# Performance work log

Measured on AMD Instinct MI355X. Metric: run time of the kernel, lower is better.

## Reference

```python
import jax, jax.numpy as jnp
import numpy as np

DIM = 384
NHEAD = 8
HD = DIM // NHEAD          # 48, rotary/pos-enc head dim
P = 3
CORR_DIM = 2 * 49 * P * P  # 882
NFRAMES = 24
PPI = 96                   # patches per frame
NPATCH = NFRAMES * PPI     # 2304 SoftAgg segments (unique kk)
E = NPATCH * NFRAMES       # 55296 edges
M = PPI                    # tokens per (i,j) group


def _linear(x, W, b):
    return x @ W + b


def _ln(x, g, b, eps=1e-3):
    mu = x.mean(-1, keepdims=True)
    var = ((x - mu) ** 2).mean(-1, keepdims=True)
    return (x - mu) * jax.lax.rsqrt(var + eps) * g + b


def _mlp2(x, W1, b1, W2, b2):
    return _linear(jax.nn.relu(_linear(x, W1, b1)), W2, b2)


@jax.custom_vjp
def grad_clip(x):
    return x

def _gc_fwd(x):
    return x, None

def _gc_bwd(_, g):
    g = jnp.where(jnp.isnan(g), jnp.zeros_like(g), g)
    return (jnp.clip(g, -0.01, 0.01),)

grad_clip.defvjp(_gc_fwd, _gc_bwd)


def _soft_agg(x, seg, Wf, bf, Wg, bg, Wh, bh):
    # x: [1,E,D]; seg: [E] contiguous segment ids in [0, NPATCH)
    g = _linear(x, Wg, bg)[0]                                    # [E,D]
    gmax = jax.ops.segment_max(g, seg, num_segments=NPATCH)
    ex = jnp.exp(g - gmax[seg])
    den = jax.ops.segment_sum(ex, seg, num_segments=NPATCH)
    w = ex / den[seg]                                            # scatter_softmax over segments
    f = _linear(x, Wf, bf)[0]
    y = jax.ops.segment_sum(f * w, seg, num_segments=NPATCH)     # [NPATCH,D]
    return _linear(y, Wh, bh)[seg][None]                         # expand back to [1,E,D]


def _rotate_half(x):
    x1, x2 = jnp.split(x, 2, axis=-1)
    return jnp.concatenate([-x2, x1], axis=-1)


def _gated_linear_attention(x, cos, sin, Wq, bq, Wk, bk, Wv, bv, Wm, bm, Wgt, bgt):
    # x: [N,M,D]; cos/sin: [N,1,M,HD] broadcast over heads
    N = x.shape[0]
    def heads(t):
        return t.reshape(N, M, NHEAD, HD).transpose(0, 2, 1, 3)  # [N,H,M,HD]
    q = heads(_linear(x, Wq, bq))
    k = heads(_linear(x, Wk, bk))
    v = heads(_linear(x, Wv, bv))
    q = q * cos + _rotate_half(q) * sin
    k = k * cos + _rotate_half(k) * sin
    Q = jax.nn.elu(q) + 1.0
    K = jax.nn.elu(k) + 1.0
    KV = jnp.einsum('nhsd,nhsv->nhdv', K, v)
    Z = 1.0 / (jnp.einsum('nhld,nhd->nhl', Q, K.sum(2)) + 1e-6)
    out = jnp.einsum('nhld,nhdv,nhl->nhlv', Q, KV, Z)
    msg = _linear(out.transpose(0, 2, 1, 3).reshape(N, M, DIM), Wm, bm)
    gate = jax.nn.sigmoid(_linear(jnp.concatenate([x, msg], -1), Wgt, bgt))
    return x + gate * msg


def _forward(net, inp, corr, posenc_cache, kk, ix, jx, ij_ind,
             Wc1, bc1, Wc2, bc2, g_lnc, b_lnc, Wc3, bc3,
             g_norm, b_norm,
             W1a, b1a, W1b, b1b, W2a, b2a, W2b, b2b,
             Wf, bf, Wg, bg, Wh, bh,
             g_norm2, b_norm2,
             Wq, bq, Wk, bk, Wv, bv, Wm, bm, Wgt, bgt,
             Wd, bd, Ww, bw):
    # corr encoder: Linear-ReLU-Linear-LN-ReLU-Linear
    c = jax.nn.relu(_linear(corr, Wc1, bc1))
    c = _ln(_linear(c, Wc2, bc2), g_lnc, b_lnc)
    c = _linear(jax.nn.relu(c), Wc3, bc3)
    net = net + inp + c
    net = _ln(net, g_norm, b_norm)
    # neighbor gather + masked MLP + residual (mask applied BEFORE the MLP, as in torch)
    mask_ix = (ix >= 0).astype(net.dtype)[None, :, None]
    mask_jx = (jx >= 0).astype(net.dtype)[None, :, None]
    net = net + _mlp2(mask_ix * net[:, ix], W1a, b1a, W1b, b1b)
    net = net + _mlp2(mask_jx * net[:, jx], W2a, b2a, W2b, b2b)
    net = net + _soft_agg(net, kk, Wf, bf, Wg, bg, Wh, bh)
    b = net.shape[0]
    flat = ij_ind.reshape(-1)
    tokens = net[:, flat, :].reshape(-1, M, DIM)                 # [N,M,D], N = E//M
    pe = posenc_cache[:, :, :, flat, :].reshape(2, tokens.shape[0], 1, M, HD)
    tokens = _ln(tokens, g_norm2, b_norm2)
    tokens = _gated_linear_attention(tokens, pe[0], pe[1], Wq, bq, Wk, bk, Wv, bv, Wm, bm, Wgt, bgt)
    tokens = tokens.reshape(b, -1, DIM)
    reverse_ind = jnp.zeros((E,), jnp.int32).at[flat].set(jnp.arange(E, dtype=jnp.int32))
    net = tokens[:, reverse_ind, :]
    d_out = grad_clip(_linear(jax.nn.relu(net), Wd, bd))
    w_out = jax.nn.sigmoid(grad_clip(_linear(jax.nn.relu(net), Ww, bw)))
    return net, d_out, w_out


def setup_inputs() -> dict:
    key = jax.random.key(0)
    ki = iter(jax.random.split(key, 80))
    # complete patch graph: each patch connects to all frames; edge id = k*NFRAMES + j
    kkn = np.repeat(np.arange(NPATCH), NFRAMES)
    iin = kkn // PPI
    jjn = np.tile(np.arange(NFRAMES), NPATCH)
    e = np.arange(E)
    ixn = np.where(jjn >= 1, e - 1, -1)                 # fastba.neighbors: same kk, jj-1
    jxn = np.where(jjn + 1 < NFRAMES, e + 1, -1)        # same kk, jj+1
    ij = iin * 12345 + jjn
    ij_ind = np.sort(np.argsort(ij, kind='stable').reshape(-1, M), axis=-1)

    def rn(shape):
        return jax.random.normal(next(ki), shape, jnp.float32)
    def W(fi, fo):
        s = 1.0 / np.sqrt(fi)
        return jax.random.uniform(next(ki), (fi, fo), jnp.float32, -s, s)
    def bvec(fi, n):
        s = 1.0 / np.sqrt(fi)
        return jax.random.uniform(next(ki), (n,), jnp.float32, -s, s)

    theta = jax.random.uniform(next(ki), (1, 1, E, HD), jnp.float32, 0.0, 2.0 * np.pi)
    posenc = jnp.stack([jnp.cos(theta), jnp.sin(theta)], axis=0)  # [2,1,1,E,HD]

    return {
        'net': rn((1, E, DIM)), 'inp': rn((1, E, DIM)),
        'corr': rn((1, E, CORR_DIM)), 'flow': rn((1, E, 2)),
        'posenc_cache': posenc,
        'ii': jnp.asarray(iin, jnp.int32), 'jj': jnp.asarray(jjn, jnp.int32),
        'kk': jnp.asarray(kkn, jnp.int32), 'ix': jnp.asarray(ixn, jnp.int32),
        'jx': jnp.asarray(jxn, jnp.int32), 'ij_ind': jnp.asarray(ij_ind, jnp.int32),
        'Wc1': W(CORR_DIM, DIM), 'bc1': bvec(CORR_DIM, DIM),
        'Wc2': W(DIM, DIM), 'bc2': bvec(DIM, DIM),
        'g_lnc': jnp.ones((DIM,), jnp.float32), 'b_lnc': jnp.zeros((DIM,), jnp.float32),
        'Wc3': W(DIM, DIM), 'bc3': bvec(DIM, DIM),
        'g_norm': jnp.ones((DIM,), jnp.float32), 'b_norm': jnp.zeros((DIM,), jnp.float32),
        'W1a': W(DIM, DIM), 'b1a': bvec(DIM, DIM), 'W1b': W(DIM, DIM), 'b1b': bvec(DIM, DIM),
        'W2a': W(DIM, DIM), 'b2a': bvec(DIM, DIM), 'W2b': W(DIM, DIM), 'b2b': bvec(DIM, DIM),
        'Wf': W(DIM, DIM), 'bf': bvec(DIM, DIM), 'Wg': W(DIM, DIM), 'bg': bvec(DIM, DIM),
        'Wh': W(DIM, DIM), 'bh': bvec(DIM, DIM),
        'g_norm2': jnp.ones((DIM,), jnp.float32), 'b_norm2': jnp.zeros((DIM,), jnp.float32),
        'Wq': W(DIM, DIM), 'bq': bvec(DIM, DIM), 'Wk': W(DIM, DIM), 'bk': bvec(DIM, DIM),
        'Wv': W(DIM, DIM), 'bv': bvec(DIM, DIM), 'Wm': W(DIM, DIM), 'bm': bvec(DIM, DIM),
        'Wgt': W(2 * DIM, DIM), 'bgt': bvec(2 * DIM, DIM),
        'Wd': W(DIM, 2), 'bd': bvec(DIM, 2), 'Ww': W(DIM, 2), 'bw': bvec(DIM, 2),
    }


def reference(net, inp, corr, flow, posenc_cache, ii, jj, kk, ix, jx, ij_ind,
              Wc1, bc1, Wc2, bc2, g_lnc, b_lnc, Wc3, bc3,
              g_norm, b_norm,
              W1a, b1a, W1b, b1b, W2a, b2a, W2b, b2b,
              Wf, bf, Wg, bg, Wh, bh,
              g_norm2, b_norm2,
              Wq, bq, Wk, bk, Wv, bv, Wm, bm, Wgt, bgt,
              Wd, bd, Ww, bw):
    return _forward(net, inp, corr, posenc_cache, kk, ix, jx, ij_ind,
                    Wc1, bc1, Wc2, bc2, g_lnc, b_lnc, Wc3, bc3,
                    g_norm, b_norm,
                    W1a, b1a, W1b, b1b, W2a, b2a, W2b, b2b,
                    Wf, bf, Wg, bg, Wh, bh,
                    g_norm2, b_norm2,
                    Wq, bq, Wk, bk, Wv, bv, Wm, bm, Wgt, bgt,
                    Wd, bd, Ww, bw)
```

## Files before the change

### kernel.cpp

```cpp
#include <hip/hip_runtime.h>
#include <math.h>

#define DIMV 384
#define NHEADV 8
#define HDV 48
#define CORR_DIMV 882
#define CORR_PAD 896
#define NFRAMESV 24
#define PPIV 96
#define NPATCHV (NFRAMESV * PPIV)
#define ETOK (NPATCHV * NFRAMESV)
#define MTOK 96
#define NGRP (ETOK / MTOK)

using f32x4 = __attribute__((ext_vector_type(4))) float;
using s16x8 = __attribute__((ext_vector_type(8))) short;
using u16x4 = __attribute__((ext_vector_type(4))) unsigned short;

__device__ __forceinline__ unsigned int f2bf(float x) {
    union { float f; unsigned int u; } c; c.f = x;
    unsigned int u = c.u;
    u += 0x7fffu + ((u >> 16) & 1u);
    return u >> 16;
}
__device__ __forceinline__ float bf2f(unsigned short x) {
    union { unsigned int u; float f; } c; c.u = ((unsigned int)x) << 16;
    return c.f;
}

__device__ __forceinline__ void gload_lds16(const void* g, void* l) {
    __builtin_amdgcn_global_load_lds(
        (const __attribute__((address_space(1))) unsigned int*)g,
        (__attribute__((address_space(3))) unsigned int*)l, 16, 0, 0);
}

__device__ __forceinline__ void xcd_tile(int& colblk, int& rowblk) {
    const int nwg  = gridDim.x * gridDim.y;
    const int flat = blockIdx.y * gridDim.x + blockIdx.x;
    const int xcd  = flat & 7;
    const int base = flat >> 3;
    const int q = nwg >> 3, r = nwg & 7;
    const int nf = (xcd < r ? xcd * (q + 1) : r * (q + 1) + (xcd - r) * q) + base;
    colblk = nf % gridDim.x;
    rowblk = nf / gridDim.x;
}

template<int EPI, bool GATHER>
__global__ __launch_bounds__(256)
void gemm_bb(const unsigned short* __restrict__ A, int lda,
             const unsigned short* __restrict__ Wt,
             const float* __restrict__ bias,
             float* __restrict__ C,
             unsigned short* __restrict__ Cb, int ldcb, int cbofs,
             const int* __restrict__ gidx,
             const unsigned short* __restrict__ zrow, int K)
{
    int colblk, rowblk;
    xcd_tile(colblk, rowblk);
    const int row0 = rowblk * 128;
    const int col0 = colblk * 128;

    __shared__ __align__(16) unsigned short As[2 * 128 * 32];
    __shared__ __align__(16) unsigned short Bs[2 * 128 * 32];

    const int tid  = threadIdx.x;
    const int lane = tid & 63;
    const int wid  = tid >> 6;
    const int wm   = wid >> 1;
    const int wn   = wid & 1;

    const int rl = lane >> 2;
    const int cp = lane & 3;

    const unsigned short* asrc[2];
    const unsigned short* bsrc[2];
    #pragma unroll
    for (int s = 0; s < 2; ++s) {
        const int r = wid * 32 + s * 16 + rl;
        const int c = cp ^ ((r >> 1) & 3);
        long arow = row0 + r;
        if (GATHER) arow = gidx[row0 + r];
        asrc[s] = (GATHER && arow < 0) ? (zrow + c * 8)
                                       : (A + arow * (long)lda + c * 8);
        bsrc[s] = Wt + (long)(col0 + r) * K + c * 8;
    }

    f32x4 acc[4][4] = {};
    const int ntiles = K >> 5;
    const int rsel = lane & 15;
    const int kq   = lane >> 4;

    auto stage = [&](int b, int ko) {
        unsigned short* a0 = &As[b * 4096 + wid * 1024];
        unsigned short* b0 = &Bs[b * 4096 + wid * 1024];
        gload_lds16(asrc[0] + ko, a0);
        gload_lds16(asrc[1] + ko, a0 + 512);
        gload_lds16(bsrc[0] + ko, b0);
        gload_lds16(bsrc[1] + ko, b0 + 512);
    };
    auto body = [&](int b) {
        const unsigned short* Ab = &As[b * 4096];
        const unsigned short* Bf = &Bs[b * 4096];
        s16x8 a[4], w[4];
        #pragma unroll
        for (int i = 0; i < 4; ++i) {
            const int R = wm * 64 + i * 16 + rsel;
            a[i] = *(const s16x8*)&Ab[R * 32 + ((kq ^ ((R >> 1) & 3)) << 3)];
        }
        #pragma unroll
        for (int j = 0; j < 4; ++j) {
            const int R = wn * 64 + j * 16 + rsel;
            w[j] = *(const s16x8*)&Bf[R * 32 + ((kq ^ ((R >> 1) & 3)) << 3)];
        }
        #pragma unroll
        for (int i = 0; i < 4; ++i)
            #pragma unroll
            for (int j = 0; j < 4; ++j)
                acc[i][j] = __builtin_amdgcn_mfma_f32_16x16x32_bf16(a[i], w[j], acc[i][j], 0, 0, 0);
    };

    stage(0, 0);
    int cur = 0;
    for (int t = 0; t + 1 < ntiles; ++t) {
        stage(cur ^ 1, (t + 1) << 5);
        asm volatile("s_waitcnt vmcnt(4)\n\ts_barrier" ::: "memory");
        body(cur);
        asm volatile("s_barrier" ::: "memory");
        cur ^= 1;
    }
    asm volatile("s_waitcnt vmcnt(0)\n\ts_barrier" ::: "memory");
    body(cur);

    const int ccol = lane & 15;
    const int rgrp = lane >> 4;
    #pragma unroll
    for (int i = 0; i < 4; ++i) {
        const long rbase = row0 + wm * 64 + i * 16 + rgrp * 4;
        #pragma unroll
        for (int j = 0; j < 4; ++j) {
            const int col = col0 + wn * 64 + j * 16 + ccol;
            const float bsv = bias ? bias[col] : 0.f;
            #pragma unroll
            for (int rr = 0; rr < 4; ++rr) {
                const long row = rbase + rr;
                float v = acc[i][j][rr] + bsv;
                if (EPI == 0) C[row * (long)DIMV + col] = v;
                if (EPI == 1) Cb[row * (long)ldcb + cbofs + col] = (unsigned short)f2bf(fmaxf(v, 0.f));
                if (EPI == 5) Cb[row * (long)ldcb + cbofs + col] = (unsigned short)f2bf(v);
                if (EPI == 6) { const long off = row * (long)ldcb + col;
                                Cb[off] = (unsigned short)f2bf(bf2f(Cb[off]) + v); }
                if (EPI == 7) {
                    const float gate = 1.f / (1.f + expf(-v));
                    const float tok  = bf2f(Cb[row * (long)ldcb + col]);
                    const float msg  = bf2f(Cb[row * (long)ldcb + cbofs + col]);
                    C[(long)gidx[row] * DIMV + col] = tok + gate * msg;
                }
            }
        }
    }
}

struct WPtrs13 { const float* p[13]; };

__global__ __launch_bounds__(256)
void wtrans13(WPtrs13 w, unsigned short* __restrict__ out)
{
    __shared__ float t[32][33];
    const float* W = w.p[blockIdx.z];
    unsigned short* O = out + (size_t)blockIdx.z * DIMV * DIMV;
    const int k0 = blockIdx.x * 32, n0 = blockIdx.y * 32;
    const int tx = threadIdx.x, ty = threadIdx.y;
    #pragma unroll
    for (int i = ty; i < 32; i += 8)
        t[i][tx] = W[(long)(k0 + i) * DIMV + n0 + tx];
    __syncthreads();
    #pragma unroll
    for (int i = ty; i < 32; i += 8)
        O[(long)(n0 + i) * DIMV + k0 + tx] = (unsigned short)f2bf(t[tx][i]);
}

__global__ __launch_bounds__(256)
void wtransb(const float* __restrict__ W, unsigned short* __restrict__ O,
             int krows, int ldo)
{
    __shared__ float t[32][33];
    const int k0 = blockIdx.x * 32, n0 = blockIdx.y * 32;
    const int tx = threadIdx.x, ty = threadIdx.y;
    #pragma unroll
    for (int i = ty; i < 32; i += 8)
        t[i][tx] = (k0 + i < krows) ? W[(long)(k0 + i) * DIMV + n0 + tx] : 0.f;
    __syncthreads();
    #pragma unroll
    for (int i = ty; i < 32; i += 8)
        O[(long)(n0 + i) * ldo + k0 + tx] = (unsigned short)f2bf(t[tx][i]);
}

__global__ __launch_bounds__(256)
void corrconv(const float* __restrict__ corr, unsigned int* __restrict__ corrb,
              unsigned int* __restrict__ zr)
{
    if (blockIdx.x == 0 && threadIdx.x < 512) zr[threadIdx.x] = 0u;
    const long idx = (long)blockIdx.x * 256 + threadIdx.x;
    if (idx >= (long)ETOK * (CORR_PAD / 2)) return;
    const long e = idx / (CORR_PAD / 2);
    const int  p = (int)(idx % (CORR_PAD / 2));
    const int  k = p * 2;
    unsigned v = 0u;
    if (k + 1 < CORR_DIMV) {
        const float2 f = *(const float2*)(corr + e * CORR_DIMV + k);
        v = f2bf(f.x) | (f2bf(f.y) << 16);
    }
    corrb[idx] = v;
}

__global__ __launch_bounds__(256)
void biascat(const float* __restrict__ bq, const float* __restrict__ bk,
             const float* __restrict__ bv, const float* __restrict__ bg,
             const float* __restrict__ bf_, float* __restrict__ bqkv,
             float* __restrict__ bgf)
{
    const int t = blockIdx.x * 256 + threadIdx.x;
    if (t < 384)       { bqkv[t] = bq[t];       bgf[t] = bg[t]; }
    else if (t < 768)  { bqkv[t] = bk[t - 384]; bgf[t] = bf_[t - 384]; }
    else if (t < 1152) { bqkv[t] = bv[t - 768]; }
}

template<int MODE, bool RELUB>
__global__ __launch_bounds__(256)
void ln_kernel(unsigned short* __restrict__ dstb, int ldb,
               const float* __restrict__ s0, const float* __restrict__ s1,
               const unsigned short* __restrict__ sb,
               const float* __restrict__ seg, const int* __restrict__ gather,
               const float* __restrict__ g, const float* __restrict__ b)
{
    const int wave = threadIdx.x >> 6;
    const int lane = threadIdx.x & 63;
    const long row = (long)blockIdx.x * 4 + wave;
    const long srow = (MODE == 2) ? (long)gather[row] : row;

    float x[6];
    float sum = 0.f;
    #pragma unroll
    for (int i = 0; i < 6; ++i) {
        int c = lane + i * 64;
        float v;
        if (MODE == 0) v = bf2f(sb[srow * DIMV + c]);
        if (MODE == 1) v = s0[srow * DIMV + c] + s1[srow * DIMV + c] + bf2f(sb[srow * DIMV + c]);
        if (MODE == 2) v = bf2f(sb[srow * DIMV + c]) + seg[(srow / NFRAMESV) * DIMV + c];
        x[i] = v; sum += v;
    }
    #pragma unroll
    for (int o = 32; o > 0; o >>= 1) sum += __shfl_xor(sum, o);
    float mu = sum * (1.f / DIMV);
    float vs = 0.f;
    #pragma unroll
    for (int i = 0; i < 6; ++i) { float d = x[i] - mu; vs += d * d; }
    #pragma unroll
    for (int o = 32; o > 0; o >>= 1) vs += __shfl_xor(vs, o);
    float rstd = rsqrtf(vs * (1.f / DIMV) + 1e-3f);
    #pragma unroll
    for (int i = 0; i < 6; ++i) {
        int c = lane + i * 64;
        float y = (x[i] - mu) * rstd * g[c] + b[c];
        dstb[row * (long)ldb + c] = (unsigned short)f2bf(RELUB ? fmaxf(y, 0.f) : y);
    }
}

__global__ __launch_bounds__(384)
void softagg_kernel(const unsigned short* __restrict__ gf,
                    unsigned short* __restrict__ yb)
{
    const int p = blockIdx.x;
    const int col = threadIdx.x;
    const long base = (long)p * NFRAMESV * 768 + col;
    float gv[NFRAMESV];
    float gmax = -INFINITY;
    #pragma unroll
    for (int r = 0; r < NFRAMESV; ++r) {
        gv[r] = bf2f(gf[base + (long)r * 768]);
        gmax = fmaxf(gmax, gv[r]);
    }
    float den = 0.f;
    #pragma unroll
    for (int r = 0; r < NFRAMESV; ++r) { gv[r] = expf(gv[r] - gmax); den += gv[r]; }
    float acc = 0.f;
    #pragma unroll
    for (int r = 0; r < NFRAMESV; ++r) acc += bf2f(gf[base + 384 + (long)r * 768]) * gv[r];
    yb[(long)p * DIMV + col] = (unsigned short)f2bf(acc / den);
}

__global__ __launch_bounds__(256)
void rope_kernel(unsigned short* __restrict__ q, unsigned short* __restrict__ k,
                 int ld, const float* __restrict__ pos, const int* __restrict__ flat)
{
    const long idx = (long)blockIdx.x * 256 + threadIdx.x;
    const long e = idx / 48;
    const int rem = (int)(idx % 48);
    const int h = rem / 6, d4 = (rem % 6) * 4;
    const int tok = flat[e];
    const float* cp = pos + (long)tok * HDV;
    const float* sp = pos + (long)ETOK * HDV + (long)tok * HDV;
    const float4 c1 = *(const float4*)(cp + d4);
    const float4 c2 = *(const float4*)(cp + d4 + 24);
    const float4 s1 = *(const float4*)(sp + d4);
    const float4 s2 = *(const float4*)(sp + d4 + 24);
    const long o1 = e * ld + h * HDV + d4;
    const long o2 = o1 + 24;

    float c1a[4] = {c1.x, c1.y, c1.z, c1.w};
    float c2a[4] = {c2.x, c2.y, c2.z, c2.w};
    float s1a[4] = {s1.x, s1.y, s1.z, s1.w};
    float s2a[4] = {s2.x, s2.y, s2.z, s2.w};

    u16x4 q1 = *(const u16x4*)&q[o1];
    u16x4 q2 = *(const u16x4*)&q[o2];
    u16x4 k1 = *(const u16x4*)&k[o1];
    u16x4 k2 = *(const u16x4*)&k[o2];
    u16x4 q1o, q2o, k1o, k2o;
    #pragma unroll
    for (int i = 0; i < 4; ++i) {
        const float qa = bf2f(q1[i]), qb = bf2f(q2[i]);
        float r1 = qa * c1a[i] - qb * s1a[i];
        float r2 = qb * c2a[i] + qa * s2a[i];
        r1 = (r1 > 0.f) ? r1 + 1.f : expf(r1);
        r2 = (r2 > 0.f) ? r2 + 1.f : expf(r2);
        q1o[i] = (unsigned short)f2bf(r1);
        q2o[i] = (unsigned short)f2bf(r2);
        const float ka = bf2f(k1[i]), kb = bf2f(k2[i]);
        float t1 = ka * c1a[i] - kb * s1a[i];
        float t2 = kb * c2a[i] + ka * s2a[i];
        t1 = (t1 > 0.f) ? t1 + 1.f : expf(t1);
        t2 = (t2 > 0.f) ? t2 + 1.f : expf(t2);
        k1o[i] = (unsigned short)f2bf(t1);
        k2o[i] = (unsigned short)f2bf(t2);
    }
    *(u16x4*)&q[o1] = q1o;
    *(u16x4*)&q[o2] = q2o;
    *(u16x4*)&k[o1] = k1o;
    *(u16x4*)&k[o2] = k2o;
}

__global__ __launch_bounds__(256)
void attn_kernel(const unsigned short* __restrict__ qb,
                 const unsigned short* __restrict__ kb,
                 const unsigned short* __restrict__ vb, int ld,
                 unsigned short* __restrict__ ob, int ldo)
{
    __shared__ unsigned short KVt[4][48][64];
    __shared__ float KsumS[4][48];
    __shared__ float ZlS[4][96];

    const int tid  = threadIdx.x;
    const int wid  = tid >> 6;
    const int lane = tid & 63;
    const int task = blockIdx.x * 4 + wid;
    const int n = task >> 3, h = task & 7;

    const long base  = ((long)n * MTOK) * ld + h * HDV;
    const long baseo = ((long)n * MTOK) * ldo + h * HDV;

    const int c16   = lane & 15;
    const int kq    = lane >> 4;
    const int khalf = kq * 8;

    if (lane < 48) {
        const int s = (lane & 7) << 3;
        const uint4 z = make_uint4(0u, 0u, 0u, 0u);
        *(uint4*)&KVt[wid][lane][48 ^ s] = z;
        *(uint4*)&KVt[wid][lane][56 ^ s] = z;
    }

    f32x4 kv[3][3] = {};
    float ksum_p[3] = {0.f, 0.f, 0.f};

    for (int ks = 0; ks < 3; ++ks) {
        const int l0 = ks * 32 + khalf;
        s16x8 afr[3], bfr[3];
        #pragma unroll
        for (int mf = 0; mf < 3; ++mf) {
            const int d = mf * 16 + c16;
            union { unsigned short us[8]; s16x8 v; } pk;
            float s = 0.f;
            #pragma unroll
            for (int j = 0; j < 8; ++j) {
                const unsigned short kw = kb[base + (long)(l0 + j) * ld + d];
                s += bf2f(kw);
                pk.us[j] = kw;
            }
            ksum_p[mf] += s;
            afr[mf] = pk.v;
        }
        #pragma unroll
        for (int nf = 0; nf < 3; ++nf) {
            const int dv = nf * 16 + c16;
            union { unsigned short us[8]; s16x8 v; } pk;
            #pragma unroll
            for (int j = 0; j < 8; ++j)
                pk.us[j] = vb[base + (long)(l0 + j) * ld + dv];
            bfr[nf] = pk.v;
        }
        #pragma unroll
        for (int mf = 0; mf < 3; ++mf)
            #pragma unroll
            for (int nf = 0; nf < 3; ++nf)
                kv[mf][nf] = __builtin_amdgcn_mfma_f32_16x16x32_bf16(afr[mf], bfr[nf], kv[mf][nf], 0, 0, 0);
    }

    #pragma unroll
    for (int mf = 0; mf < 3; ++mf) {
        float s = ksum_p[mf];
        s += __shfl_xor(s, 16);
        s += __shfl_xor(s, 32);
        if (kq == 0) KsumS[wid][mf * 16 + c16] = s;
    }

    #pragma unroll
    for (int mf = 0; mf < 3; ++mf) {
        #pragma unroll
        for (int nf = 0; nf < 3; ++nf) {
            const int dv = nf * 16 + c16;
            const int d0 = (mf * 16 + kq * 4) ^ ((dv & 7) << 3);
            uint2 w;
            w.x = f2bf(kv[mf][nf][0]) | (f2bf(kv[mf][nf][1]) << 16);
            w.y = f2bf(kv[mf][nf][2]) | (f2bf(kv[mf][nf][3]) << 16);
            *(uint2*)&KVt[wid][dv][d0] = w;
        }
    }

    s16x8 qf[6][2];
    const s16x8 zfrag = {0, 0, 0, 0, 0, 0, 0, 0};
    #pragma unroll
    for (int mf = 0; mf < 6; ++mf) {
        const int l = mf * 16 + c16;
        float dsum = 0.f;
        #pragma unroll
        for (int ks = 0; ks < 2; ++ks) {
            if (ks == 0 || kq < 2) {
                const int d = ks * 32 + khalf;
                union { unsigned short us[8]; s16x8 v; } pk;
                pk.v = *(const s16x8*)&qb[base + (long)l * ld + d];
                #pragma unroll
                for (int j = 0; j < 8; ++j)
                    dsum += bf2f(pk.us[j]) * KsumS[wid][d + j];
                qf[mf][ks] = pk.v;
            } else {
                qf[mf][ks] = zfrag;
            }
        }
        dsum += __shfl_xor(dsum, 16);
        dsum += __shfl_xor(dsum, 32);
        if (kq == 0) ZlS[wid][l] = 1.f / (dsum + 1e-6f);
    }

    #pragma unroll
    for (int nf = 0; nf < 3; ++nf) {
        const int dv = nf * 16 + c16;
        const int sw = (dv & 7) << 3;
        const s16x8 b0 = *(const s16x8*)&KVt[wid][dv][khalf ^ sw];
        const s16x8 b1 = *(const s16x8*)&KVt[wid][dv][(32 + khalf) ^ sw];
        #pragma unroll
        for (int mf = 0; mf < 6; ++mf) {
            f32x4 a = {};
            a = __builtin_amdgcn_mfma_f32_16x16x32_bf16(qf[mf][0], b0, a, 0, 0, 0);
            a = __builtin_amdgcn_mfma_f32_16x16x32_bf16(qf[mf][1], b1, a, 0, 0, 0);
            const int lb = mf * 16 + kq * 4;
            const long rbase = baseo + (long)lb * ldo + dv;
            #pragma unroll
            for (int rr = 0; rr < 4; ++rr) {
                const float z = ZlS[wid][lb + rr];
                ob[rbase + (long)rr * ldo] = (unsigned short)f2bf(a[rr] * z);
            }
        }
    }
}

__global__ __launch_bounds__(256)
void head_kernel(const float* __restrict__ net,
                 const float* __restrict__ Wd, const float* __restrict__ bd,
                 const float* __restrict__ Ww, const float* __restrict__ bw,
                 float* __restrict__ dout, float* __restrict__ wout)
{
    const int wave = threadIdx.x >> 6;
    const int lane = threadIdx.x & 63;
    const long row = (long)blockIdx.x * 4 + wave;
    const float* p = net + row * DIMV;
    float a0 = 0.f, a1 = 0.f, a2 = 0.f, a3 = 0.f;
    #pragma unroll
    for (int i = 0; i < 6; ++i) {
        int c = lane + i * 64;
        float r = fmaxf(p[c], 0.f);
        a0 = fmaf(r, Wd[c * 2 + 0], a0);
        a1 = fmaf(r, Wd[c * 2 + 1], a1);
        a2 = fmaf(r, Ww[c * 2 + 0], a2);
        a3 = fmaf(r, Ww[c * 2 + 1], a3);
    }
    #pragma unroll
    for (int o = 32; o > 0; o >>= 1) {
        a0 += __shfl_xor(a0, o);
        a1 += __shfl_xor(a1, o);
        a2 += __shfl_xor(a2, o);
        a3 += __shfl_xor(a3, o);
    }
    if (lane == 0) {
        dout[row * 2 + 0] = a0 + bd[0];
        dout[row * 2 + 1] = a1 + bd[1];
        wout[row * 2 + 0] = 1.f / (1.f + expf(-(a2 + bw[0])));
        wout[row * 2 + 1] = 1.f / (1.f + expf(-(a3 + bw[1])));
    }
}

extern "C" void kernel_launch(void* const* d_in, const int* in_sizes, int n_in,
                              void* d_out, int out_size, void* d_ws, size_t ws_size,
                              hipStream_t stream)
{
    const float* net_in = (const float*)d_in[0];
    const float* inp    = (const float*)d_in[1];
    const float* corr   = (const float*)d_in[2];
    const float* posenc = (const float*)d_in[4];
    const int*   ix     = (const int*)d_in[8];
    const int*   jx     = (const int*)d_in[9];
    const int*   flat   = (const int*)d_in[10];

    const float* Wc1 = (const float*)d_in[11]; const float* bc1 = (const float*)d_in[12];
    const float* Wc2 = (const float*)d_in[13]; const float* bc2 = (const float*)d_in[14];
    const float* g_lnc = (const float*)d_in[15]; const float* b_lnc = (const float*)d_in[16];
    const float* Wc3 = (const float*)d_in[17]; const float* bc3 = (const float*)d_in[18];
    const float* g_norm = (const float*)d_in[19]; const float* b_norm = (const float*)d_in[20];
    const float* W1a = (const float*)d_in[21]; const float* b1a = (const float*)d_in[22];
    const float* W1b = (const float*)d_in[23]; const float* b1b = (const float*)d_in[24];
    const float* W2a = (const float*)d_in[25]; const float* b2a = (const float*)d_in[26];
    const float* W2b = (const float*)d_in[27]; const float* b2b = (const float*)d_in[28];
    const float* Wf = (const float*)d_in[29]; const float* bff = (const float*)d_in[30];
    const float* Wg = (const float*)d_in[31]; const float* bg = (const float*)d_in[32];
    const float* Wh = (const float*)d_in[33]; const float* bh = (const float*)d_in[34];
    const float* g_norm2 = (const float*)d_in[35]; const float* b_norm2 = (const float*)d_in[36];
    const float* Wq = (const float*)d_in[37]; const float* bq = (const float*)d_in[38];
    const float* Wk = (const float*)d_in[39]; const float* bk = (const float*)d_in[40];
    const float* Wv = (const float*)d_in[41]; const float* bv = (const float*)d_in[42];
    const float* Wm = (const float*)d_in[43]; const float* bm = (const float*)d_in[44];
    const float* Wgt = (const float*)d_in[45]; const float* bgt = (const float*)d_in[46];
    const float* Wd = (const float*)d_in[47]; const float* bd = (const float*)d_in[48];
    const float* Ww = (const float*)d_in[49]; const float* bw = (const float*)d_in[50];

    const size_t EB  = (size_t)ETOK * DIMV;
    const size_t WSLOT = (size_t)DIMV * DIMV;
    char* p = (char*)d_ws;
    float* Y2f = (float*)p;           p += (size_t)NPATCHV * DIMV * 4;
    unsigned short* WT = (unsigned short*)p;
    p += (13 * WSLOT + (size_t)DIMV * CORR_PAD + (size_t)DIMV * 768) * 2;
    unsigned short* ZR  = (unsigned short*)p; p += 4096;
    float* bqkv = (float*)p;          p += 1152 * 4;
    float* bgf  = (float*)p;          p += 768 * 4;
    unsigned short* Cb0 = (unsigned short*)p; p += EB * 2;
    unsigned short* Bb  = (unsigned short*)p; p += EB * 2;
    unsigned short* Xb1 = (unsigned short*)p; p += EB * 2;
    unsigned short* Xb2 = (unsigned short*)p; p += EB * 2;
    unsigned short* Xgf = (unsigned short*)p; p += (size_t)ETOK * 768 * 2;
    unsigned short* TM  = (unsigned short*)p; p += (size_t)ETOK * 768 * 2;
    unsigned short* Yb  = (unsigned short*)p; p += (size_t)NPATCHV * DIMV * 2;
    unsigned short* QKV = (unsigned short*)p; p += (size_t)ETOK * 1152 * 2;
    unsigned short* corrb = QKV;

    unsigned short* Wc2t = WT + 0 * WSLOT;
    unsigned short* Wc3t = WT + 1 * WSLOT;
    unsigned short* W1at = WT + 2 * WSLOT;
    unsigned short* W1bt = WT + 3 * WSLOT;
    unsigned short* W2at = WT + 4 * WSLOT;
    unsigned short* W2bt = WT + 5 * WSLOT;
    unsigned short* WgfT = WT + 6 * WSLOT;
    unsigned short* Wht  = WT + 8 * WSLOT;
    unsigned short* Wqkv = WT + 9 * WSLOT;
    unsigned short* Wmt  = WT + 12 * WSLOT;
    unsigned short* Wc1t = WT + 13 * WSLOT;
    unsigned short* Wgtt = Wc1t + (size_t)DIMV * CORR_PAD;

    float* out_net = (float*)d_out;
    float* out_d = out_net + EB;
    float* out_w = out_d + (size_t)ETOK * 2;

    const dim3 gB(DIMV / 128, ETOK / 128);
    const dim3 gGF(768 / 128, ETOK / 128);
    const dim3 gQKV(1152 / 128, ETOK / 128);
    const dim3 gY(DIMV / 128, NPATCHV / 128);
    const int lnBlocks = ETOK / 4;

    {
        const long tot = (long)ETOK * (CORR_PAD / 2);
        corrconv<<<(int)((tot + 255) / 256), 256, 0, stream>>>(corr, (unsigned int*)corrb, (unsigned int*)ZR);
    }
    {
        WPtrs13 w;
        w.p[0] = Wc2; w.p[1] = Wc3; w.p[2] = W1a; w.p[3] = W1b; w.p[4] = W2a;
        w.p[5] = W2b; w.p[6] = Wg;  w.p[7] = Wf;  w.p[8] = Wh;  w.p[9] = Wq;
        w.p[10] = Wk; w.p[11] = Wv; w.p[12] = Wm;
        wtrans13<<<dim3(12, 12, 13), dim3(32, 8), 0, stream>>>(w, WT);
        wtransb<<<dim3(28, 12), dim3(32, 8), 0, stream>>>(Wc1, Wc1t, CORR_DIMV, CORR_PAD);
        wtransb<<<dim3(24, 12), dim3(32, 8), 0, stream>>>(Wgt, Wgtt, 768, 768);
        biascat<<<5, 256, 0, stream>>>(bq, bk, bv, bg, bff, bqkv, bgf);
    }

    gemm_bb<1, false><<<gB, 256, 0, stream>>>(corrb, CORR_PAD, Wc1t, bc1, nullptr, Cb0, DIMV, 0, nullptr, ZR, CORR_PAD);
    gemm_bb<5, false><<<gB, 256, 0, stream>>>(Cb0, DIMV, Wc2t, bc2, nullptr, Xb1, DIMV, 0, nullptr, ZR, DIMV);
    ln_kernel<0, true><<<lnBlocks, 256, 0, stream>>>(Cb0, DIMV, nullptr, nullptr, Xb1, nullptr, nullptr, g_lnc, b_lnc);
    gemm_bb<5, false><<<gB, 256, 0, stream>>>(Cb0, DIMV, Wc3t, bc3, nullptr, Xb2, DIMV, 0, nullptr, ZR, DIMV);

    ln_kernel<1, false><<<lnBlocks, 256, 0, stream>>>(Bb, DIMV, net_in, inp, Xb2, nullptr, nullptr, g_norm, b_norm);

    gemm_bb<1, true><<<gB, 256, 0, stream>>>(Bb, DIMV, W1at, b1a, nullptr, Cb0, DIMV, 0, ix, ZR, DIMV);
    gemm_bb<6, false><<<gB, 256, 0, stream>>>(Cb0, DIMV, W1bt, b1b, nullptr, Bb, DIMV, 0, nullptr, ZR, DIMV);

    gemm_bb<1, true><<<gB, 256, 0, stream>>>(Bb, DIMV, W2at, b2a, nullptr, Cb0, DIMV, 0, jx, ZR, DIMV);
    gemm_bb<6, false><<<gB, 256, 0, stream>>>(Cb0, DIMV, W2bt, b2b, nullptr, Bb, DIMV, 0, nullptr, ZR, DIMV);

    gemm_bb<5, false><<<gGF, 256, 0, stream>>>(Bb, DIMV, WgfT, bgf, nullptr, Xgf, 768, 0, nullptr, ZR, DIMV);
    softagg_kernel<<<NPATCHV, 384, 0, stream>>>(Xgf, Yb);
    gemm_bb<0, false><<<gY, 256, 0, stream>>>(Yb, DIMV, Wht, bh, Y2f, nullptr, DIMV, 0, nullptr, ZR, DIMV);

    ln_kernel<2, false><<<lnBlocks, 256, 0, stream>>>(TM, 768, nullptr, nullptr, Bb, Y2f, flat, g_norm2, b_norm2);

    gemm_bb<5, false><<<gQKV, 256, 0, stream>>>(TM, 768, Wqkv, bqkv, nullptr, QKV, 1152, 0, nullptr, ZR, DIMV);

    rope_kernel<<<(int)((long)ETOK * 48 / 256), 256, 0, stream>>>(QKV, QKV + 384, 1152, posenc, flat);

    attn_kernel<<<NGRP * NHEADV / 4, 256, 0, stream>>>(QKV, QKV + 384, QKV + 768, 1152, Cb0, DIMV);

    gemm_bb<5, false><<<gB, 256, 0, stream>>>(Cb0, DIMV, Wmt, bm, nullptr, TM, 768, 384, nullptr, ZR, DIMV);

    gemm_bb<7, false><<<gB, 256, 0, stream>>>(TM, 768, Wgtt, bgt, out_net, TM, 768, 384, flat, ZR, 768);

    head_kernel<<<lnBlocks, 256, 0, stream>>>(out_net, Wd, bd, Ww, bw, out_d, out_w);
}
```

Baseline: 882.5 us.

## Fuse back-to-back MLP GEMM pairs into a single kernel with LDS-resident hidden

```diff
diff --git a/kernel.cpp b/kernel.cpp
--- a/kernel.cpp
+++ b/kernel.cpp
@@ -154,6 +154,147 @@
                     const float tok  = bf2f(Cb[row * (long)ldcb + col]);
                     const float msg  = bf2f(Cb[row * (long)ldcb + cbofs + col]);
                     C[(long)gidx[row] * DIMV + col] = tok + gate * msg;
+                }
+            }
+        }
+    }
+}
+
+template<int EPI2, bool GATHER>
+__global__ __launch_bounds__(512, 4)
+void fused2(const unsigned short* __restrict__ A, int lda, int K1,
+            const int* __restrict__ gidx, const unsigned short* __restrict__ zrow,
+            const unsigned short* __restrict__ Wa, const float* __restrict__ ba,
+            const unsigned short* __restrict__ Wb, const float* __restrict__ bb,
+            const unsigned short* __restrict__ prevB,
+            unsigned short* __restrict__ outB)
+{
+    __shared__ __align__(16) unsigned short Abuf[2][64 * 32];
+    __shared__ __align__(16) unsigned short H[64 * 384];
+
+    const int tid  = threadIdx.x;
+    const int lane = tid & 63;
+    const int wid  = tid >> 6;
+    const int wm   = wid & 1;
+    const int wn   = wid >> 1;
+    const int row0 = blockIdx.x * 64;
+
+    const int c16 = lane & 15;
+    const int kq  = lane >> 4;
+
+    const unsigned short* asrc = nullptr;
+    int adst = 0;
+    if (tid < 256) {
+        const int r = tid >> 2;
+        const int c = (tid & 3) ^ ((r >> 1) & 3);
+        long srow = row0 + r;
+        if (GATHER) srow = gidx[row0 + r];
+        asrc = (GATHER && srow < 0) ? (zrow + c * 8) : (A + srow * (long)lda + c * 8);
+        adst = tid * 8;
+    }
+
+    f32x4 acc[2][6] = {};
+    s16x8 wf0[6], wf1[6];
+
+    auto loadW = [&](const unsigned short* W, int K, s16x8* wf, int t) {
+        #pragma unroll
+        for (int j = 0; j < 6; ++j) {
+            const int n = wn * 96 + j * 16 + c16;
+            wf[j] = *(const s16x8*)&W[(long)n * K + t * 32 + kq * 8];
+        }
+    };
+    auto stageA = [&](int b, int t) {
+        if (tid < 256) gload_lds16(asrc + t * 32, &Abuf[b][adst]);
+    };
+    auto mfmaT = [&](int b, s16x8* wf) {
+        s16x8 a[2];
+        #pragma unroll
+        for (int i = 0; i < 2; ++i) {
+            const int R = wm * 32 + i * 16 + c16;
+            a[i] = *(const s16x8*)&Abuf[b][R * 32 + ((kq ^ ((R >> 1) & 3)) << 3)];
+        }
+        #pragma unroll
+        for (int i = 0; i < 2; ++i)
+            #pragma unroll
+            for (int j = 0; j < 6; ++j)
+                acc[i][j] = __builtin_amdgcn_mfma_f32_16x16x32_bf16(a[i], wf[j], acc[i][j], 0, 0, 0);
+    };
+    auto mfmaH = [&](int t, s16x8* wf) {
+        s16x8 a[2];
+        #pragma unroll
+        for (int i = 0; i < 2; ++i) {
+            const int R = wm * 32 + i * 16 + c16;
+            const int chunk = t * 4 + kq;
+            a[i] = *(const s16x8*)&H[R * 384 + ((chunk ^ (R & 7)) << 3)];
+        }
+        #pragma unroll
+        for (int i = 0; i < 2; ++i)
+            #pragma unroll
+            for (int j = 0; j < 6; ++j)
+                acc[i][j] = __builtin_amdgcn_mfma_f32_16x16x32_bf16(a[i], wf[j], acc[i][j], 0, 0, 0);
+    };
+
+    const int nt1 = K1 >> 5;
+    stageA(0, 0); loadW(Wa, K1, wf0, 0);
+    for (int t = 0; t < nt1; t += 2) {
+        stageA(1, t + 1); loadW(Wa, K1, wf1, t + 1);
+        asm volatile("s_waitcnt vmcnt(6)\n\ts_barrier" ::: "memory");
+        mfmaT(0, wf0);
+        asm volatile("s_barrier" ::: "memory");
+        if (t + 2 < nt1) {
+            stageA(0, t + 2); loadW(Wa, K1, wf0, t + 2);
+            asm volatile("s_waitcnt vmcnt(6)\n\ts_barrier" ::: "memory");
+        } else {
+            asm volatile("s_waitcnt vmcnt(0)\n\ts_barrier" ::: "memory");
+        }
+        mfmaT(1, wf1);
+        asm volatile("s_barrier" ::: "memory");
+    }
+
+    {
+        const int rgrp = lane >> 4;
+        #pragma unroll
+        for (int i = 0; i < 2; ++i) {
+            #pragma unroll
+            for (int j = 0; j < 6; ++j) {
+                const int col = wn * 96 + j * 16 + c16;
+                const float bav = ba[col];
+                #pragma unroll
+                for (int rr = 0; rr < 4; ++rr) {
+                    const int r = wm * 32 + i * 16 + rgrp * 4 + rr;
+                    const float v = fmaxf(acc[i][j][rr] + bav, 0.f);
+                    H[r * 384 + (((col >> 3) ^ (r & 7)) << 3) + (col & 7)] =
+                        (unsigned short)f2bf(v);
+                    acc[i][j][rr] = 0.f;
+                }
+            }
+        }
+    }
+    asm volatile("s_waitcnt lgkmcnt(0)\n\ts_barrier" ::: "memory");
+
+    loadW(Wb, 384, wf0, 0);
+    #pragma unroll 1
+    for (int t = 0; t < 12; t += 2) {
+        loadW(Wb, 384, wf1, t + 1);
+        mfmaH(t, wf0);
+        if (t + 2 < 12) loadW(Wb, 384, wf0, t + 2);
+        mfmaH(t + 1, wf1);
+    }
+
+    {
+        const int rgrp = lane >> 4;
+        #pragma unroll
+        for (int i = 0; i < 2; ++i) {
+            #pragma unroll
+            for (int j = 0; j < 6; ++j) {
+                const int col = wn * 96 + j * 16 + c16;
+                const float bbv = bb[col];
+                #pragma unroll
+                for (int rr = 0; rr < 4; ++rr) {
+                    const long R = row0 + wm * 32 + i * 16 + rgrp * 4 + rr;
+                    float v = acc[i][j][rr] + bbv;
+                    if (EPI2 == 6) v += bf2f(prevB[R * 384 + col]);
+                    outB[R * 384 + col] = (unsigned short)f2bf(v);
                 }
             }
         }
@@ -583,6 +724,7 @@
     const dim3 gQKV(1152 / 128, ETOK / 128);
     const dim3 gY(DIMV / 128, NPATCHV / 128);
     const int lnBlocks = ETOK / 4;
+    const int fBlocks  = ETOK / 64;
 
     {
         const long tot = (long)ETOK * (CORR_PAD / 2);
@@ -599,18 +741,17 @@
         biascat<<<5, 256, 0, stream>>>(bq, bk, bv, bg, bff, bqkv, bgf);
     }
 
-    gemm_bb<1, false><<<gB, 256, 0, stream>>>(corrb, CORR_PAD, Wc1t, bc1, nullptr, Cb0, DIMV, 0, nullptr, ZR, CORR_PAD);
-    gemm_bb<5, false><<<gB, 256, 0, stream>>>(Cb0, DIMV, Wc2t, bc2, nullptr, Xb1, DIMV, 0, nullptr, ZR, DIMV);
+    fused2<5, false><<<fBlocks, 512, 0, stream>>>(corrb, CORR_PAD, CORR_PAD, nullptr, ZR,
+                                                  Wc1t, bc1, Wc2t, bc2, nullptr, Xb1);
     ln_kernel<0, true><<<lnBlocks, 256, 0, stream>>>(Cb0, DIMV, nullptr, nullptr, Xb1, nullptr, nullptr, g_lnc, b_lnc);
     gemm_bb<5, false><<<gB, 256, 0, stream>>>(Cb0, DIMV, Wc3t, bc3, nullptr, Xb2, DIMV, 0, nullptr, ZR, DIMV);
 
     ln_kernel<1, false><<<lnBlocks, 256, 0, stream>>>(Bb, DIMV, net_in, inp, Xb2, nullptr, nullptr, g_norm, b_norm);
 
-    gemm_bb<1, true><<<gB, 256, 0, stream>>>(Bb, DIMV, W1at, b1a, nullptr, Cb0, DIMV, 0, ix, ZR, DIMV);
-    gemm_bb<6, false><<<gB, 256, 0, stream>>>(Cb0, DIMV, W1bt, b1b, nullptr, Bb, DIMV, 0, nullptr, ZR, DIMV);
-
-    gemm_bb<1, true><<<gB, 256, 0, stream>>>(Bb, DIMV, W2at, b2a, nullptr, Cb0, DIMV, 0, jx, ZR, DIMV);
-    gemm_bb<6, false><<<gB, 256, 0, stream>>>(Cb0, DIMV, W2bt, b2b, nullptr, Bb, DIMV, 0, nullptr, ZR, DIMV);
+    fused2<6, true><<<fBlocks, 512, 0, stream>>>(Bb, DIMV, DIMV, ix, ZR,
+                                                 W1at, b1a, W1bt, b1b, Bb, Xb1);
+    fused2<6, true><<<fBlocks, 512, 0, stream>>>(Xb1, DIMV, DIMV, jx, ZR,
+                                                 W2at, b2a, W2bt, b2b, Xb1, Bb);
 
     gemm_bb<5, false><<<gGF, 256, 0, stream>>>(Bb, DIMV, WgfT, bgf, nullptr, Xgf, 768, 0, nullptr, ZR, DIMV);
     softagg_kernel<<<NPATCHV, 384, 0, stream>>>(Xgf, Yb);
```

After: 1.512 ms. 71.4% more time.

## Fuse corr fp32-to-bf16 conversion into first GEMM and head into final epilogue

Applied to the files above, without the earlier changes.

```diff
diff --git a/kernel.cpp b/kernel.cpp
--- a/kernel.cpp
+++ b/kernel.cpp
@@ -53,7 +53,9 @@
              float* __restrict__ C,
              unsigned short* __restrict__ Cb, int ldcb, int cbofs,
              const int* __restrict__ gidx,
-             const unsigned short* __restrict__ zrow, int K)
+             const unsigned short* __restrict__ zrow, int K,
+             const float* __restrict__ Wd2, const float* __restrict__ Ww2,
+             float* __restrict__ hdw)
 {
     int colblk, rowblk;
     xcd_tile(colblk, rowblk);
@@ -133,6 +135,48 @@
 
     const int ccol = lane & 15;
     const int rgrp = lane >> 4;
+
+    if (EPI == 7) {
+        #pragma unroll
+        for (int i = 0; i < 4; ++i) {
+            #pragma unroll
+            for (int rr = 0; rr < 4; ++rr) {
+                const long row  = row0 + wm * 64 + i * 16 + rgrp * 4 + rr;
+                const long orow = gidx[row];
+                float p0 = 0.f, p1 = 0.f, p2 = 0.f, p3 = 0.f;
+                #pragma unroll
+                for (int j = 0; j < 4; ++j) {
+                    const int col = col0 + wn * 64 + j * 16 + ccol;
+                    const float v = acc[i][j][rr] + bias[col];
+                    const float gate = 1.f / (1.f + expf(-v));
+                    const float tok  = bf2f(Cb[row * (long)ldcb + col]);
+                    const float msg  = bf2f(Cb[row * (long)ldcb + cbofs + col]);
+                    const float o = tok + gate * msg;
+                    C[orow * DIMV + col] = o;
+                    const float rl_ = fmaxf(o, 0.f);
+                    p0 += rl_ * Wd2[col * 2 + 0];
+                    p1 += rl_ * Wd2[col * 2 + 1];
+                    p2 += rl_ * Ww2[col * 2 + 0];
+                    p3 += rl_ * Ww2[col * 2 + 1];
+                }
+                #pragma unroll
+                for (int o = 8; o > 0; o >>= 1) {
+                    p0 += __shfl_xor(p0, o);
+                    p1 += __shfl_xor(p1, o);
+                    p2 += __shfl_xor(p2, o);
+                    p3 += __shfl_xor(p3, o);
+                }
+                if (ccol == 0) {
+                    atomicAdd(&hdw[orow * 4 + 0], p0);
+                    atomicAdd(&hdw[orow * 4 + 1], p1);
+                    atomicAdd(&hdw[orow * 4 + 2], p2);
+                    atomicAdd(&hdw[orow * 4 + 3], p3);
+                }
+            }
+        }
+        return;
+    }
+
     #pragma unroll
     for (int i = 0; i < 4; ++i) {
         const long rbase = row0 + wm * 64 + i * 16 + rgrp * 4;
@@ -149,12 +193,133 @@
                 if (EPI == 5) Cb[row * (long)ldcb + cbofs + col] = (unsigned short)f2bf(v);
                 if (EPI == 6) { const long off = row * (long)ldcb + col;
                                 Cb[off] = (unsigned short)f2bf(bf2f(Cb[off]) + v); }
-                if (EPI == 7) {
-                    const float gate = 1.f / (1.f + expf(-v));
-                    const float tok  = bf2f(Cb[row * (long)ldcb + col]);
-                    const float msg  = bf2f(Cb[row * (long)ldcb + cbofs + col]);
-                    C[(long)gidx[row] * DIMV + col] = tok + gate * msg;
-                }
+            }
+        }
+    }
+}
+
+__global__ __launch_bounds__(256)
+void gemm_f32a(const float* __restrict__ A,
+               const unsigned short* __restrict__ Wt,
+               const float* __restrict__ bias,
+               unsigned short* __restrict__ Cb)
+{
+    int colblk, rowblk;
+    xcd_tile(colblk, rowblk);
+    const int row0 = rowblk * 128;
+    const int col0 = colblk * 128;
+
+    __shared__ __align__(16) unsigned short As[2 * 128 * 32];
+    __shared__ __align__(16) unsigned short Bs[2 * 128 * 32];
+
+    const int tid  = threadIdx.x;
+    const int lane = tid & 63;
+    const int wid  = tid >> 6;
+    const int wm   = wid >> 1;
+    const int wn   = wid & 1;
+
+    const int ra = tid >> 1;
+    const int kh = (tid & 1) << 4;
+    const float* arow = A + (long)(row0 + ra) * CORR_DIMV;
+
+    const int rl = lane >> 2;
+    const int cp = lane & 3;
+    const unsigned short* bsrc[2];
+    #pragma unroll
+    for (int s = 0; s < 2; ++s) {
+        const int r = wid * 32 + s * 16 + rl;
+        const int c = cp ^ ((r >> 1) & 3);
+        bsrc[s] = Wt + (long)(col0 + r) * CORR_PAD + c * 8;
+    }
+
+    f32x4 acc[4][4] = {};
+    const int ntiles = CORR_PAD >> 5;
+    const int rsel = lane & 15;
+    const int kq   = lane >> 4;
+
+    float2 ar[8];
+
+    auto loadA = [&](int t) {
+        const int k0 = (t << 5) + kh;
+        #pragma unroll
+        for (int j = 0; j < 8; ++j) {
+            const int k = k0 + j * 2;
+            ar[j] = (k < CORR_DIMV) ? *(const float2*)(arow + k)
+                                    : make_float2(0.f, 0.f);
+        }
+    };
+    auto writeA = [&](int b) {
+        unsigned int w[8];
+        #pragma unroll
+        for (int j = 0; j < 8; ++j)
+            w[j] = f2bf(ar[j].x) | (f2bf(ar[j].y) << 16);
+        const int cbase = kh >> 3;
+        const int sw = (ra >> 1) & 3;
+        unsigned short* dst = &As[b * 4096 + ra * 32];
+        *(uint4*)&dst[((cbase ^ sw) << 3)]       = make_uint4(w[0], w[1], w[2], w[3]);
+        *(uint4*)&dst[(((cbase + 1) ^ sw) << 3)] = make_uint4(w[4], w[5], w[6], w[7]);
+    };
+    auto stageW = [&](int b, int t) {
+        const int ko = t << 5;
+        unsigned short* b0 = &Bs[b * 4096 + wid * 1024];
+        gload_lds16(bsrc[0] + ko, b0);
+        gload_lds16(bsrc[1] + ko, b0 + 512);
+    };
+    auto body = [&](int b) {
+        const unsigned short* Ab = &As[b * 4096];
+        const unsigned short* Bf = &Bs[b * 4096];
+        s16x8 a[4], w[4];
+        #pragma unroll
+        for (int i = 0; i < 4; ++i) {
+            const int R = wm * 64 + i * 16 + rsel;
+            a[i] = *(const s16x8*)&Ab[R * 32 + ((kq ^ ((R >> 1) & 3)) << 3)];
+        }
+        #pragma unroll
+        for (int j = 0; j < 4; ++j) {
+            const int R = wn * 64 + j * 16 + rsel;
+            w[j] = *(const s16x8*)&Bf[R * 32 + ((kq ^ ((R >> 1) & 3)) << 3)];
+        }
+        #pragma unroll
+        for (int i = 0; i < 4; ++i)
+            #pragma unroll
+            for (int j = 0; j < 4; ++j)
+                acc[i][j] = __builtin_amdgcn_mfma_f32_16x16x32_bf16(a[i], w[j], acc[i][j], 0, 0, 0);
+    };
+
+    loadA(0);
+    stageW(0, 0);
+    asm volatile("s_waitcnt vmcnt(2)" ::: "memory");
+    writeA(0);
+
+    int cur = 0;
+    for (int t = 0; t < ntiles; ++t) {
+        if (t + 1 < ntiles) {
+            loadA(t + 1);
+            asm volatile("s_waitcnt vmcnt(8) lgkmcnt(0)\n\ts_barrier" ::: "memory");
+            stageW(cur ^ 1, t + 1);
+            body(cur);
+            asm volatile("s_waitcnt vmcnt(2)" ::: "memory");
+            writeA(cur ^ 1);
+        } else {
+            asm volatile("s_waitcnt vmcnt(0) lgkmcnt(0)\n\ts_barrier" ::: "memory");
+            body(cur);
+        }
+        cur ^= 1;
+    }
+
+    const int ccol = lane & 15;
+    const int rgrp = lane >> 4;
+    #pragma unroll
+    for (int i = 0; i < 4; ++i) {
+        const long rbase = row0 + wm * 64 + i * 16 + rgrp * 4;
+        #pragma unroll
+        for (int j = 0; j < 4; ++j) {
+            const int col = col0 + wn * 64 + j * 16 + ccol;
+            const float bsv = bias[col];
+            #pragma unroll
+            for (int rr = 0; rr < 4; ++rr) {
+                const float v = acc[i][j][rr] + bsv;
+                Cb[(rbase + rr) * (long)DIMV + col] = (unsigned short)f2bf(fmaxf(v, 0.f));
             }
         }
     }
@@ -196,30 +361,13 @@
 }
 
 __global__ __launch_bounds__(256)
-void corrconv(const float* __restrict__ corr, unsigned int* __restrict__ corrb,
-              unsigned int* __restrict__ zr)
-{
-    if (blockIdx.x == 0 && threadIdx.x < 512) zr[threadIdx.x] = 0u;
-    const long idx = (long)blockIdx.x * 256 + threadIdx.x;
-    if (idx >= (long)ETOK * (CORR_PAD / 2)) return;
-    const long e = idx / (CORR_PAD / 2);
-    const int  p = (int)(idx % (CORR_PAD / 2));
-    const int  k = p * 2;
-    unsigned v = 0u;
-    if (k + 1 < CORR_DIMV) {
-        const float2 f = *(const float2*)(corr + e * CORR_DIMV + k);
-        v = f2bf(f.x) | (f2bf(f.y) << 16);
-    }
-    corrb[idx] = v;
-}
-
-__global__ __launch_bounds__(256)
 void biascat(const float* __restrict__ bq, const float* __restrict__ bk,
              const float* __restrict__ bv, const float* __restrict__ bg,
              const float* __restrict__ bf_, float* __restrict__ bqkv,
-             float* __restrict__ bgf)
+             float* __restrict__ bgf, unsigned int* __restrict__ zr)
 {
     const int t = blockIdx.x * 256 + threadIdx.x;
+    if (t < 1024) zr[t] = 0u;
     if (t < 384)       { bqkv[t] = bq[t];       bgf[t] = bg[t]; }
     else if (t < 768)  { bqkv[t] = bk[t - 384]; bgf[t] = bf_[t - 384]; }
     else if (t < 1152) { bqkv[t] = bv[t - 768]; }
@@ -475,38 +623,15 @@
 }
 
 __global__ __launch_bounds__(256)
-void head_kernel(const float* __restrict__ net,
-                 const float* __restrict__ Wd, const float* __restrict__ bd,
-                 const float* __restrict__ Ww, const float* __restrict__ bw,
-                 float* __restrict__ dout, float* __restrict__ wout)
-{
-    const int wave = threadIdx.x >> 6;
-    const int lane = threadIdx.x & 63;
-    const long row = (long)blockIdx.x * 4 + wave;
-    const float* p = net + row * DIMV;
-    float a0 = 0.f, a1 = 0.f, a2 = 0.f, a3 = 0.f;
-    #pragma unroll
-    for (int i = 0; i < 6; ++i) {
-        int c = lane + i * 64;
-        float r = fmaxf(p[c], 0.f);
-        a0 = fmaf(r, Wd[c * 2 + 0], a0);
-        a1 = fmaf(r, Wd[c * 2 + 1], a1);
-        a2 = fmaf(r, Ww[c * 2 + 0], a2);
-        a3 = fmaf(r, Ww[c * 2 + 1], a3);
-    }
-    #pragma unroll
-    for (int o = 32; o > 0; o >>= 1) {
-        a0 += __shfl_xor(a0, o);
-        a1 += __shfl_xor(a1, o);
-        a2 += __shfl_xor(a2, o);
-        a3 += __shfl_xor(a3, o);
-    }
-    if (lane == 0) {
-        dout[row * 2 + 0] = a0 + bd[0];
-        dout[row * 2 + 1] = a1 + bd[1];
-        wout[row * 2 + 0] = 1.f / (1.f + expf(-(a2 + bw[0])));
-        wout[row * 2 + 1] = 1.f / (1.f + expf(-(a3 + bw[1])));
-    }
+void head_fin(const float* __restrict__ hdw,
+              const float* __restrict__ bd, const float* __restrict__ bw,
+              float* __restrict__ dout, float* __restrict__ wout)
+{
+    const long r = (long)blockIdx.x * 256 + threadIdx.x;
+    dout[r * 2 + 0] = hdw[r * 4 + 0] + bd[0];
+    dout[r * 2 + 1] = hdw[r * 4 + 1] + bd[1];
+    wout[r * 2 + 0] = 1.f / (1.f + expf(-(hdw[r * 4 + 2] + bw[0])));
+    wout[r * 2 + 1] = 1.f / (1.f + expf(-(hdw[r * 4 + 3] + bw[1])));
 }
 
 extern "C" void kernel_launch(void* const* d_in, const int* in_sizes, int n_in,
@@ -559,7 +684,7 @@
     unsigned short* TM  = (unsigned short*)p; p += (size_t)ETOK * 768 * 2;
     unsigned short* Yb  = (unsigned short*)p; p += (size_t)NPATCHV * DIMV * 2;
     unsigned short* QKV = (unsigned short*)p; p += (size_t)ETOK * 1152 * 2;
-    unsigned short* corrb = QKV;
+    float* hdw = (float*)p;           p += (size_t)ETOK * 4 * 4;
 
     unsigned short* Wc2t = WT + 0 * WSLOT;
     unsigned short* Wc3t = WT + 1 * WSLOT;
@@ -585,10 +710,6 @@
     const int lnBlocks = ETOK / 4;
 
     {
-        const long tot = (long)ETOK * (CORR_PAD / 2);
-        corrconv<<<(int)((tot + 255) / 256), 256, 0, stream>>>(corr, (unsigned int*)corrb, (unsigned int*)ZR);
-    }
-    {
         WPtrs13 w;
         w.p[0] = Wc2; w.p[1] = Wc3; w.p[2] = W1a; w.p[3] = W1b; w.p[4] = W2a;
         w.p[5] = W2b; w.p[6] = Wg;  w.p[7] = Wf;  w.p[8] = Wh;  w.p[9] = Wq;
@@ -596,37 +717,38 @@
         wtrans13<<<dim3(12, 12, 13), dim3(32, 8), 0, stream>>>(w, WT);
         wtransb<<<dim3(28, 12), dim3(32, 8), 0, stream>>>(Wc1, Wc1t, CORR_DIMV, CORR_PAD);
         wtransb<<<dim3(24, 12), dim3(32, 8), 0, stream>>>(Wgt, Wgtt, 768, 768);
-        biascat<<<5, 256, 0, stream>>>(bq, bk, bv, bg, bff, bqkv, bgf);
-    }
-
-    gemm_bb<1, false><<<gB, 256, 0, stream>>>(corrb, CORR_PAD, Wc1t, bc1, nullptr, Cb0, DIMV, 0, nullptr, ZR, CORR_PAD);
-    gemm_bb<5, false><<<gB, 256, 0, stream>>>(Cb0, DIMV, Wc2t, bc2, nullptr, Xb1, DIMV, 0, nullptr, ZR, DIMV);
+        biascat<<<5, 256, 0, stream>>>(bq, bk, bv, bg, bff, bqkv, bgf, (unsigned int*)ZR);
+        hipMemsetAsync(hdw, 0, (size_t)ETOK * 4 * sizeof(float), stream);
+    }
+
+    gemm_f32a<<<gB, 256, 0, stream>>>(corr, Wc1t, bc1, Cb0);
+    gemm_bb<5, false><<<gB, 256, 0, stream>>>(Cb0, DIMV, Wc2t, bc2, nullptr, Xb1, DIMV, 0, nullptr, ZR, DIMV, nullptr, nullptr, nullptr);
     ln_kernel<0, true><<<lnBlocks, 256, 0, stream>>>(Cb0, DIMV, nullptr, nullptr, Xb1, nullptr, nullptr, g_lnc, b_lnc);
-    gemm_bb<5, false><<<gB, 256, 0, stream>>>(Cb0, DIMV, Wc3t, bc3, nullptr, Xb2, DIMV, 0, nullptr, ZR, DIMV);
+    gemm_bb<5, false><<<gB, 256, 0, stream>>>(Cb0, DIMV, Wc3t, bc3, nullptr, Xb2, DIMV, 0, nullptr, ZR, DIMV, nullptr, nullptr, nullptr);
 
     ln_kernel<1, false><<<lnBlocks, 256, 0, stream>>>(Bb, DIMV, net_in, inp, Xb2, nullptr, nullptr, g_norm, b_norm);
 
-    gemm_bb<1, true><<<gB, 256, 0, stream>>>(Bb, DIMV, W1at, b1a, nullptr, Cb0, DIMV, 0, ix, ZR, DIMV);
-    gemm_bb<6, false><<<gB, 256, 0, stream>>>(Cb0, DIMV, W1bt, b1b, nullptr, Bb, DIMV, 0, nullptr, ZR, DIMV);
-
-    gemm_bb<1, true><<<gB, 256, 0, stream>>>(Bb, DIMV, W2at, b2a, nullptr, Cb0, DIMV, 0, jx, ZR, DIMV);
-    gemm_bb<6, false><<<gB, 256, 0, stream>>>(Cb0, DIMV, W2bt, b2b, nullptr, Bb, DIMV, 0, nullptr, ZR, DIMV);
-
-    gemm_bb<5, false><<<gGF, 256, 0, stream>>>(Bb, DIMV, WgfT, bgf, nullptr, Xgf, 768, 0, nullptr, ZR, DIMV);
+    gemm_bb<1, true><<<gB, 256, 0, stream>>>(Bb, DIMV, W1at, b1a, nullptr, Cb0, DIMV, 0, ix, ZR, DIMV, nullptr, nullptr, nullptr);
+    gemm_bb<6, false><<<gB, 256, 0, stream>>>(Cb0, DIMV, W1bt, b1b, nullptr, Bb, DIMV, 0, nullptr, ZR, DIMV, nullptr, nullptr, nullptr);
+
+    gemm_bb<1, true><<<gB, 256, 0, stream>>>(Bb, DIMV, W2at, b2a, nullptr, Cb0, DIMV, 0, jx, ZR, DIMV, nullptr, nullptr, nullptr);
+    gemm_bb<6, false><<<gB, 256, 0, stream>>>(Cb0, DIMV, W2bt, b2b, nullptr, Bb, DIMV, 0, nullptr, ZR, DIMV, nullptr, nullptr, nullptr);
+
+    gemm_bb<5, false><<<gGF, 256, 0, stream>>>(Bb, DIMV, WgfT, bgf, nullptr, Xgf, 768, 0, nullptr, ZR, DIMV, nullptr, nullptr, nullptr);
     softagg_kernel<<<NPATCHV, 384, 0, stream>>>(Xgf, Yb);
-    gemm_bb<0, false><<<gY, 256, 0, stream>>>(Yb, DIMV, Wht, bh, Y2f, nullptr, DIMV, 0, nullptr, ZR, DIMV);
+    gemm_bb<0, false><<<gY, 256, 0, stream>>>(Yb, DIMV, Wht, bh, Y2f, nullptr, DIMV, 0, nullptr, ZR, DIMV, nullptr, nullptr, nullptr);
 
     ln_kernel<2, false><<<lnBlocks, 256, 0, stream>>>(TM, 768, nullptr, nullptr, Bb, Y2f, flat, g_norm2, b_norm2);
 
-    gemm_bb<5, false><<<gQKV, 256, 0, stream>>>(TM, 768, Wqkv, bqkv, nullptr, QKV, 1152, 0, nullptr, ZR, DIMV);
+    gemm_bb<5, false><<<gQKV, 256, 0, stream>>>(TM, 768, Wqkv, bqkv, nullptr, QKV, 1152, 0, nullptr, ZR, DIMV, nullptr, nullptr, nullptr);
 
     rope_kernel<<<(int)((long)ETOK * 48 / 256), 256, 0, stream>>>(QKV, QKV + 384, 1152, posenc, flat);
 
     attn_kernel<<<NGRP * NHEADV / 4, 256, 0, stream>>>(QKV, QKV + 384, QKV + 768, 1152, Cb0, DIMV);
 
-    gemm_bb<5, false><<<gB, 256, 0, stream>>>(Cb0, DIMV, Wmt, bm, nullptr, TM, 768, 384, nullptr, ZR, DIMV);
-
-    gemm_bb<7, false><<<gB, 256, 0, stream>>>(TM, 768, Wgtt, bgt, out_net, TM, 768, 384, flat, ZR, 768);
-
-    head_kernel<<<lnBlocks, 256, 0, stream>>>(out_net, Wd, bd, Ww, bw, out_d, out_w);
-}
+    gemm_bb<5, false><<<gB, 256, 0, stream>>>(Cb0, DIMV, Wmt, bm, nullptr, TM, 768, 384, nullptr, ZR, DIMV, nullptr, nullptr, nullptr);
+
+    gemm_bb<7, false><<<gB, 256, 0, stream>>>(TM, 768, Wgtt, bgt, out_net, TM, 768, 384, flat, ZR, 768, Wd, Ww, hdw);
+
+    head_fin<<<ETOK / 256, 256, 0, stream>>>(hdw, bd, bw, out_d, out_w);
+}
```

New measurement: 982.9 us. 11.4% more time.
